# Kernel tuning notes

Measured on AMD Instinct MI355X. Metric: run time of the kernel, lower is better.

The kernel has to match this reference:

```python
import jax, jax.numpy as jnp
import numpy as np

# Model dims: N = polynomial degree, RANK = CP rank, HxW image, S = flattened size
N, RANK, H, W = 4, 128, 256, 256
S = H * W
B = 32
EPS = 1e-5  # torch BatchNorm2d default eps


def setup_inputs() -> dict:
    key = jax.random.key(0)
    ks = jax.random.split(key, 4)
    x = jax.random.normal(ks[0], (B, 1, H, W), dtype=jnp.float32)
    # PolyLayer (PolyGAN CCP) parameters: per-degree factors U_n [S, RANK],
    # output projection C [S, RANK], output bias beta [S]
    U = jax.random.normal(ks[1], (N, S, RANK), dtype=jnp.float32) * 0.02
    C = jax.random.normal(ks[2], (S, RANK), dtype=jnp.float32) * 0.02
    beta = jax.random.normal(ks[3], (S,), dtype=jnp.float32) * 0.02
    # BatchNorm2d(1) affine params (torch default init: weight=1, bias=0)
    gamma = jnp.ones((1,), dtype=jnp.float32)
    bn_bias = jnp.zeros((1,), dtype=jnp.float32)
    return {"x": x, "U": U, "C": C, "beta": beta, "gamma": gamma, "bn_bias": bn_bias}


def reference(x, U, C, beta, gamma, bn_bias):
    b = x.shape[0]
    # BatchNorm2d(num_features=1), training mode: biased batch stats over (N,H,W)
    mean = jnp.mean(x, axis=(0, 2, 3), keepdims=True)
    var = jnp.var(x, axis=(0, 2, 3), keepdims=True)
    xn = (x - mean) * jax.lax.rsqrt(var + EPS)
    xn = xn * gamma.reshape(1, -1, 1, 1) + bn_bias.reshape(1, -1, 1, 1)
    # Flatten each sample: [B, S]. The torch Generator applies PolyLayer
    # per-sample across Python threads; here it is one batched call.
    z = xn.reshape(b, S)
    # CCP polynomial: t_n = U_n^T z for each degree -> [N, B, RANK]
    t = jnp.einsum('bs,nsr->nbr', z, U)
    h = t[0]
    for n in range(1, N):  # fixed small degree loop (structural, not data dim)
        h = t[n] * h + h   # h_n = (U_n^T z) * h_{n-1} + h_{n-1}
    out = h @ C.T + beta   # project back to image space: [B, S]
    return out.reshape(b, 1, H, W)
```

## Files before the change

kernel.cpp:

```cpp
#include <hip/hip_runtime.h>

#define SDIM 65536
#define BDIM 32
#define RDIM 128
#define NDEG 4
#define NCHUNK 512
#define CHUNK_S (SDIM / NCHUNK)
#define MTOT (BDIM * SDIM)
#define EPS_BN 1e-5f
#define NSTATB 512

__global__ void k_stats(const float* __restrict__ x, float* __restrict__ partial) {
    __shared__ float s_sum[256];
    __shared__ float s_sq[256];
    int tid = threadIdx.x;
    int gid = blockIdx.x * 256 + tid;
    int stride = gridDim.x * 256;
    float sum = 0.f, sq = 0.f;
    const float4* x4 = (const float4*)x;
    for (int i = gid; i < MTOT / 4; i += stride) {
        float4 v = x4[i];
        sum += (v.x + v.y) + (v.z + v.w);
        sq  += (v.x * v.x + v.y * v.y) + (v.z * v.z + v.w * v.w);
    }
    s_sum[tid] = sum; s_sq[tid] = sq;
    __syncthreads();
    for (int off = 128; off > 0; off >>= 1) {
        if (tid < off) { s_sum[tid] += s_sum[tid + off]; s_sq[tid] += s_sq[tid + off]; }
        __syncthreads();
    }
    if (tid == 0) { partial[blockIdx.x * 2] = s_sum[0]; partial[blockIdx.x * 2 + 1] = s_sq[0]; }
}

__global__ void k_stats_fin(const float* __restrict__ partial, float* __restrict__ stats) {
    __shared__ float s_sum[256];
    __shared__ float s_sq[256];
    int tid = threadIdx.x;
    float sum = partial[tid * 2] + partial[(tid + 256) * 2];
    float sq  = partial[tid * 2 + 1] + partial[(tid + 256) * 2 + 1];
    s_sum[tid] = sum; s_sq[tid] = sq;
    __syncthreads();
    for (int off = 128; off > 0; off >>= 1) {
        if (tid < off) { s_sum[tid] += s_sum[tid + off]; s_sq[tid] += s_sq[tid + off]; }
        __syncthreads();
    }
    if (tid == 0) { stats[0] = s_sum[0]; stats[1] = s_sq[0]; }
}

__global__ void __launch_bounds__(256) k_norm_t(const float* __restrict__ x,
                                                const float* __restrict__ gamma,
                                                const float* __restrict__ bnb,
                                                const float* __restrict__ stats,
                                                float* __restrict__ zT) {
    __shared__ float lds[64][33];
    int tid = threadIdx.x;
    int s0 = blockIdx.x * 64;
    float mean = stats[0] * (1.f / MTOT);
    float var  = stats[1] * (1.f / MTOT) - mean * mean;
    float istd = rsqrtf(var + EPS_BN);
    float a  = gamma[0] * istd;
    float c0 = bnb[0] - mean * a;

    int sl = tid & 63, bq = tid >> 6;
#pragma unroll
    for (int k = 0; k < 8; ++k) {
        int b = k * 4 + bq;
        lds[sl][b] = fmaf(a, x[(size_t)b * SDIM + s0 + sl], c0);
    }
    __syncthreads();
    int bl = tid & 31, sq = tid >> 5;
#pragma unroll
    for (int k = 0; k < 8; ++k) {
        int s = k * 8 + sq;
        zT[(size_t)(s0 + s) * BDIM + bl] = lds[s][bl];
    }
}

__global__ void __launch_bounds__(256) k_gemm_t(const float* __restrict__ zT,
                                                const float* __restrict__ U,
                                                float* __restrict__ t_part) {
    __shared__ float lds_z[CHUNK_S * BDIM];
    int tid  = threadIdx.x;
    int p    = tid & 31;
    int o    = tid >> 5;
    int chunk = blockIdx.x;
    int n     = blockIdx.y;
    int s0 = chunk * CHUNK_S;

    {
        const float4* src4 = (const float4*)(zT + (size_t)s0 * BDIM);
        float4* dst4 = (float4*)lds_z;
#pragma unroll
        for (int i = 0; i < (CHUNK_S * BDIM / 4) / 256; ++i)
            dst4[i * 256 + tid] = src4[i * 256 + tid];
    }
    __syncthreads();

    const float* Ub = U + (size_t)n * SDIM * RDIM + (size_t)s0 * RDIM;
    const float4* zq = (const float4*)lds_z;

    float acc[4][4];
#pragma unroll
    for (int j = 0; j < 4; ++j)
#pragma unroll
        for (int k = 0; k < 4; ++k) acc[j][k] = 0.f;

    for (int ss = 0; ss < CHUNK_S; ss += 4) {
        float4 u[4], z[4];
#pragma unroll
        for (int k = 0; k < 4; ++k) {
            u[k] = *(const float4*)(Ub + (size_t)(ss + k) * RDIM + 4 * p);
            z[k] = zq[(ss + k) * (BDIM / 4) + o];
        }
#pragma unroll
        for (int k = 0; k < 4; ++k) {
            acc[0][0] = fmaf(z[k].x, u[k].x, acc[0][0]);
            acc[0][1] = fmaf(z[k].x, u[k].y, acc[0][1]);
            acc[0][2] = fmaf(z[k].x, u[k].z, acc[0][2]);
            acc[0][3] = fmaf(z[k].x, u[k].w, acc[0][3]);
            acc[1][0] = fmaf(z[k].y, u[k].x, acc[1][0]);
            acc[1][1] = fmaf(z[k].y, u[k].y, acc[1][1]);
            acc[1][2] = fmaf(z[k].y, u[k].z, acc[1][2]);
            acc[1][3] = fmaf(z[k].y, u[k].w, acc[1][3]);
            acc[2][0] = fmaf(z[k].z, u[k].x, acc[2][0]);
            acc[2][1] = fmaf(z[k].z, u[k].y, acc[2][1]);
            acc[2][2] = fmaf(z[k].z, u[k].z, acc[2][2]);
            acc[2][3] = fmaf(z[k].z, u[k].w, acc[2][3]);
            acc[3][0] = fmaf(z[k].w, u[k].x, acc[3][0]);
            acc[3][1] = fmaf(z[k].w, u[k].y, acc[3][1]);
            acc[3][2] = fmaf(z[k].w, u[k].z, acc[3][2]);
            acc[3][3] = fmaf(z[k].w, u[k].w, acc[3][3]);
        }
    }

    float* outp = t_part + ((size_t)n * NCHUNK + chunk) * (BDIM * RDIM);
#pragma unroll
    for (int j = 0; j < 4; ++j) {
        int b = o * 4 + j;
        *(float4*)(outp + b * RDIM + 4 * p) =
            make_float4(acc[j][0], acc[j][1], acc[j][2], acc[j][3]);
    }
}

__global__ void __launch_bounds__(256) k_reduce_h(const float* __restrict__ t_part,
                                                  float* __restrict__ h) {
    __shared__ float lds[NDEG][8][32];
    int tid = threadIdx.x;
    int il = tid & 31;
    int cg = tid >> 5;
    int i0 = blockIdx.x * 32;

#pragma unroll
    for (int n = 0; n < NDEG; ++n) {
        float s = 0.f;
#pragma unroll 8
        for (int k = 0; k < 64; ++k) {
            int c = cg * 64 + k;
            s += t_part[(size_t)(n * NCHUNK + c) * (BDIM * RDIM) + i0 + il];
        }
        lds[n][cg][il] = s;
    }
    __syncthreads();
    if (tid < 32) {
        float t[NDEG];
#pragma unroll
        for (int n = 0; n < NDEG; ++n) {
            float s = 0.f;
#pragma unroll
            for (int g = 0; g < 8; ++g) s += lds[n][g][il];
            t[n] = s;
        }
        float hh = t[0];
#pragma unroll
        for (int n = 1; n < NDEG; ++n) hh = fmaf(t[n], hh, hh);
        h[i0 + il] = hh;
    }
}

__global__ void __launch_bounds__(256) k_out(const float* __restrict__ h,
                                             const float* __restrict__ Cm,
                                             const float* __restrict__ beta,
                                             float* __restrict__ out) {
    int tid = threadIdx.x;
    int s   = (blockIdx.x >> 1) * 64 + (tid & 63);
    int bg  = __builtin_amdgcn_readfirstlane((blockIdx.x & 1) * 4 + (tid >> 6));
    int b0  = bg * 4;

    float acc[4] = {0.f, 0.f, 0.f, 0.f};
    const float4* Cr = (const float4*)(Cm + (size_t)s * RDIM);
    const float* hb = h + b0 * RDIM;

#pragma unroll 8
    for (int rc = 0; rc < RDIM / 4; ++rc) {
        float4 c = Cr[rc];
#pragma unroll
        for (int j = 0; j < 4; ++j) {
            const float* hr = hb + j * RDIM + rc * 4;
            float a = acc[j];
            a = fmaf(c.x, hr[0], a);
            a = fmaf(c.y, hr[1], a);
            a = fmaf(c.z, hr[2], a);
            a = fmaf(c.w, hr[3], a);
            acc[j] = a;
        }
    }
    float bt = beta[s];
#pragma unroll
    for (int j = 0; j < 4; ++j)
        out[(size_t)(b0 + j) * SDIM + s] = acc[j] + bt;
}

extern "C" void kernel_launch(void* const* d_in, const int* in_sizes, int n_in,
                              void* d_out, int out_size, void* d_ws, size_t ws_size,
                              hipStream_t stream) {
    const float* x     = (const float*)d_in[0];
    const float* U     = (const float*)d_in[1];
    const float* Cm    = (const float*)d_in[2];
    const float* beta  = (const float*)d_in[3];
    const float* gamma = (const float*)d_in[4];
    const float* bnb   = (const float*)d_in[5];
    float* out = (float*)d_out;

    char* ws = (char*)d_ws;
    size_t off = 0;
    float* stats   = (float*)(ws + off); off += 256;
    float* partial = (float*)(ws + off); off += NSTATB * 2 * 4;
    float* zT      = (float*)(ws + off); off += (size_t)BDIM * SDIM * 4;
    float* t_part  = (float*)(ws + off); off += (size_t)NDEG * NCHUNK * BDIM * RDIM * 4;
    float* h       = (float*)(ws + off); off += (size_t)BDIM * RDIM * 4;

    k_stats<<<NSTATB, 256, 0, stream>>>(x, partial);
    k_stats_fin<<<1, 256, 0, stream>>>(partial, stats);
    k_norm_t<<<SDIM / 64, 256, 0, stream>>>(x, gamma, bnb, stats, zT);
    dim3 g3(NCHUNK, NDEG);
    k_gemm_t<<<g3, 256, 0, stream>>>(zT, U, t_part);
    k_reduce_h<<<128, 256, 0, stream>>>(t_part, h);
    k_out<<<2048, 256, 0, stream>>>(h, Cm, beta, out);
}
```

Measured before the change: 111.9 us.

## Stage U tiles into LDS with double-buffered global_load_lds in projection GEMM

The U-projection GEMM now copies 16-row tiles of U straight into shared memory with the asynchronous global-to-LDS load instruction. It double-buffers them so the next tile's fetch overlaps the FMAs on the current tile. Before, all eight 32-lane groups of a block loaded the same U rows from global memory, relying on cache for reuse. The change adds a barrier per 16-row step and extra shared-memory use, which may lower occupancy.

```diff
diff --git a/kernel.cpp b/kernel.cpp
--- a/kernel.cpp
+++ b/kernel.cpp
@@ -6,9 +6,12 @@
 #define NDEG 4
 #define NCHUNK 512
 #define CHUNK_S (SDIM / NCHUNK)
+#define NSTEP (CHUNK_S / 16)
 #define MTOT (BDIM * SDIM)
 #define EPS_BN 1e-5f
 #define NSTATB 512
+
+typedef float f32x4 __attribute__((ext_vector_type(4)));
 
 __global__ void k_stats(const float* __restrict__ x, float* __restrict__ partial) {
     __shared__ float s_sum[256];
@@ -76,28 +79,51 @@
     }
 }
 
+#define FMA16(zz, uu) \
+    acc[0][0]=fmaf((zz).x,(uu).x,acc[0][0]); acc[0][1]=fmaf((zz).x,(uu).y,acc[0][1]); \
+    acc[0][2]=fmaf((zz).x,(uu).z,acc[0][2]); acc[0][3]=fmaf((zz).x,(uu).w,acc[0][3]); \
+    acc[1][0]=fmaf((zz).y,(uu).x,acc[1][0]); acc[1][1]=fmaf((zz).y,(uu).y,acc[1][1]); \
+    acc[1][2]=fmaf((zz).y,(uu).z,acc[1][2]); acc[1][3]=fmaf((zz).y,(uu).w,acc[1][3]); \
+    acc[2][0]=fmaf((zz).z,(uu).x,acc[2][0]); acc[2][1]=fmaf((zz).z,(uu).y,acc[2][1]); \
+    acc[2][2]=fmaf((zz).z,(uu).z,acc[2][2]); acc[2][3]=fmaf((zz).z,(uu).w,acc[2][3]); \
+    acc[3][0]=fmaf((zz).w,(uu).x,acc[3][0]); acc[3][1]=fmaf((zz).w,(uu).y,acc[3][1]); \
+    acc[3][2]=fmaf((zz).w,(uu).z,acc[3][2]); acc[3][3]=fmaf((zz).w,(uu).w,acc[3][3]);
+
+#define GLL(gp, lp) __builtin_amdgcn_global_load_lds( \
+    (const __attribute__((address_space(1))) void*)(gp), \
+    (__attribute__((address_space(3))) void*)(lp), 16, 0, 0)
+
 __global__ void __launch_bounds__(256) k_gemm_t(const float* __restrict__ zT,
                                                 const float* __restrict__ U,
                                                 float* __restrict__ t_part) {
-    __shared__ float lds_z[CHUNK_S * BDIM];
+    __shared__ float z_lds[CHUNK_S * BDIM];
+    __shared__ float u_lds[2][16 * RDIM];
     int tid  = threadIdx.x;
     int p    = tid & 31;
     int o    = tid >> 5;
+    int wv   = tid >> 6;
+    int ln   = tid & 63;
     int chunk = blockIdx.x;
     int n     = blockIdx.y;
     int s0 = chunk * CHUNK_S;
 
     {
         const float4* src4 = (const float4*)(zT + (size_t)s0 * BDIM);
-        float4* dst4 = (float4*)lds_z;
+        float4* dst4 = (float4*)z_lds;
 #pragma unroll
         for (int i = 0; i < (CHUNK_S * BDIM / 4) / 256; ++i)
             dst4[i * 256 + tid] = src4[i * 256 + tid];
     }
-    __syncthreads();
-
-    const float* Ub = U + (size_t)n * SDIM * RDIM + (size_t)s0 * RDIM;
-    const float4* zq = (const float4*)lds_z;
+
+    const float* Ut = U + (size_t)n * SDIM * RDIM + (size_t)s0 * RDIM;
+
+    {
+        const float* gp = Ut + (size_t)(4 * wv) * RDIM + ln * 4;
+        float* lp = &u_lds[0][4 * wv * RDIM];
+        GLL(gp, lp);
+        GLL(gp + 256, lp + 256);
+    }
+    __syncthreads();
 
     float acc[4][4];
 #pragma unroll
@@ -105,32 +131,22 @@
 #pragma unroll
         for (int k = 0; k < 4; ++k) acc[j][k] = 0.f;
 
-    for (int ss = 0; ss < CHUNK_S; ss += 4) {
-        float4 u[4], z[4];
-#pragma unroll
-        for (int k = 0; k < 4; ++k) {
-            u[k] = *(const float4*)(Ub + (size_t)(ss + k) * RDIM + 4 * p);
-            z[k] = zq[(ss + k) * (BDIM / 4) + o];
-        }
-#pragma unroll
-        for (int k = 0; k < 4; ++k) {
-            acc[0][0] = fmaf(z[k].x, u[k].x, acc[0][0]);
-            acc[0][1] = fmaf(z[k].x, u[k].y, acc[0][1]);
-            acc[0][2] = fmaf(z[k].x, u[k].z, acc[0][2]);
-            acc[0][3] = fmaf(z[k].x, u[k].w, acc[0][3]);
-            acc[1][0] = fmaf(z[k].y, u[k].x, acc[1][0]);
-            acc[1][1] = fmaf(z[k].y, u[k].y, acc[1][1]);
-            acc[1][2] = fmaf(z[k].y, u[k].z, acc[1][2]);
-            acc[1][3] = fmaf(z[k].y, u[k].w, acc[1][3]);
-            acc[2][0] = fmaf(z[k].z, u[k].x, acc[2][0]);
-            acc[2][1] = fmaf(z[k].z, u[k].y, acc[2][1]);
-            acc[2][2] = fmaf(z[k].z, u[k].z, acc[2][2]);
-            acc[2][3] = fmaf(z[k].z, u[k].w, acc[2][3]);
-            acc[3][0] = fmaf(z[k].w, u[k].x, acc[3][0]);
-            acc[3][1] = fmaf(z[k].w, u[k].y, acc[3][1]);
-            acc[3][2] = fmaf(z[k].w, u[k].z, acc[3][2]);
-            acc[3][3] = fmaf(z[k].w, u[k].w, acc[3][3]);
-        }
+    for (int t = 0; t < NSTEP; ++t) {
+        if (t + 1 < NSTEP) {
+            const float* gp = Ut + (size_t)((t + 1) * 16 + 4 * wv) * RDIM + ln * 4;
+            float* lp = &u_lds[(t + 1) & 1][4 * wv * RDIM];
+            GLL(gp, lp);
+            GLL(gp + 256, lp + 256);
+        }
+        const float* ub = u_lds[t & 1];
+        const float* zb = z_lds + (size_t)(t * 16) * BDIM;
+#pragma unroll
+        for (int rr = 0; rr < 16; ++rr) {
+            f32x4 u4 = *(const f32x4*)(ub + rr * RDIM + 4 * p);
+            f32x4 z4 = *(const f32x4*)(zb + rr * BDIM + 4 * o);
+            FMA16(z4, u4)
+        }
+        __syncthreads();
     }
 
     float* outp = t_part + ((size_t)n * NCHUNK + chunk) * (BDIM * RDIM);
```

Result: faster. 107.9 us (-3.6%).
